# Performance work log

Hardware: AMD Instinct MI355X
Metric: run time of the kernel (lower is better)

Reference implementation:

```python
import jax, jax.numpy as jnp
import numpy as np

V, E, R, L = 50257, 256, 1024, 4
B, T = 32, 512
LN_EPS = 1e-5


def setup_inputs() -> dict:
    key = jax.random.key(0)
    ks = jax.random.split(key, 6)
    x = jax.random.randint(ks[0], (B, T), 0, V)
    embed = jax.random.normal(ks[1], (V, E), dtype=jnp.float32)
    # torch init: randn(in, out) / sqrt(in) / 0.9
    Win0 = jax.random.normal(ks[2], (E, R), dtype=jnp.float32) / np.sqrt(E).astype(np.float32) / 0.9
    Win_rest = jax.random.normal(ks[3], (L - 1, R, R), dtype=jnp.float32) / np.sqrt(R).astype(np.float32) / 0.9
    R_stack = jax.random.normal(ks[4], (L, R, R), dtype=jnp.float32) / np.sqrt(R).astype(np.float32) / 0.9
    gamma = jnp.ones((R * L,), dtype=jnp.float32)
    beta = jnp.zeros((R * L,), dtype=jnp.float32)
    return {"x": x, "embed": embed, "Win0": Win0, "Win_rest": Win_rest,
            "R_stack": R_stack, "gamma": gamma, "beta": beta}


def _layer_norm(h, gamma, beta):
    mu = jnp.mean(h, axis=-1, keepdims=True)
    var = jnp.mean(jnp.square(h - mu), axis=-1, keepdims=True)
    return (h - mu) * jax.lax.rsqrt(var + LN_EPS) * gamma + beta


def reference(x, embed, Win0, Win_rest, R_stack, gamma, beta):
    # x: [B,T] int ids. deep_type='deep_esn': layer i>0 takes the *current-step*
    # state of layer i-1 as input; readout concatenates all layer states.
    xe = embed[x]                      # [B,T,E]
    xe = jnp.transpose(xe, (1, 0, 2))  # [T,B,E] for scan over time
    b = x.shape[0]
    n_layers = R_stack.shape[0]
    r = R_stack.shape[1]
    init = tuple(jnp.zeros((b, r), dtype=xe.dtype) for _ in range(n_layers))

    def step(states, emb_t):
        new_states = []
        inp = emb_t
        for i in range(n_layers):
            W = Win0 if i == 0 else Win_rest[i - 1]
            s = jnp.tanh(states[i] @ R_stack[i] + inp @ W)  # [B,R]
            new_states.append(s)
            inp = s  # deep stacking: feed updated state to next layer
        return tuple(new_states), None

    final_states, _ = jax.lax.scan(step, init, xe)
    h = jnp.concatenate(final_states, axis=-1)  # [B, R*L]
    return _layer_norm(h, gamma, beta)
```

## Files before the change

kernel.cpp:

```cpp
#include <hip/hip_runtime.h>
#include <math.h>


#define TT    512
#define RDIM  1024
#define EDIM  256
#define NL    4
#define BB    32
#define NBLK  256
#define JW    16
#define HDIM  (RDIM * NL)
#define NPAN  4
#define CSTRIDE 32

#define S_ELEMS   (2 * NL * NPAN * RDIM * 8)
#define FIN_ELEMS (BB * HDIM)

typedef float vf2 __attribute__((ext_vector_type(2)));
typedef float vf4 __attribute__((ext_vector_type(4)));

__device__ __forceinline__ float dpp_xor1(float x) {
    return __int_as_float(__builtin_amdgcn_mov_dpp(__float_as_int(x), 0xB1, 0xF, 0xF, true));
}
__device__ __forceinline__ float dpp_xor2(float x) {
    return __int_as_float(__builtin_amdgcn_mov_dpp(__float_as_int(x), 0x4E, 0xF, 0xF, true));
}

__device__ __forceinline__ void gload_sc(vf4& d, const void* p) {
    asm volatile("global_load_dwordx4 %0, %1, off sc0 sc1" : "=v"(d) : "v"(p));
}
__device__ __forceinline__ void gload_pl(vf4& d, const void* p) {
    asm volatile("global_load_dwordx4 %0, %1, off" : "=v"(d) : "v"(p));
}
__device__ __forceinline__ void vwait(int wn, vf4& r) {
    if (wn >= 7)      asm volatile("s_waitcnt vmcnt(7)" : "+v"(r));
    else if (wn == 6) asm volatile("s_waitcnt vmcnt(6)" : "+v"(r));
    else if (wn == 5) asm volatile("s_waitcnt vmcnt(5)" : "+v"(r));
    else if (wn == 4) asm volatile("s_waitcnt vmcnt(4)" : "+v"(r));
    else if (wn == 3) asm volatile("s_waitcnt vmcnt(3)" : "+v"(r));
    else if (wn == 2) asm volatile("s_waitcnt vmcnt(2)" : "+v"(r));
    else if (wn == 1) asm volatile("s_waitcnt vmcnt(1)" : "+v"(r));
    else              asm volatile("s_waitcnt vmcnt(0)" : "+v"(r));
}

__global__ void gather_kernel(const int* __restrict__ x,
                              const float* __restrict__ embed,
                              float* __restrict__ xe)
{
    __shared__ int   ids[BB];
    __shared__ float sh[BB * (EDIM + 1)];
    const int t = blockIdx.x, tid = threadIdx.x;
    if (tid < BB) ids[tid] = x[tid * TT + t];
    __syncthreads();
    for (int r = 0; r < BB; ++r)
        sh[r * (EDIM + 1) + tid] = embed[ids[r] * EDIM + tid];
    __syncthreads();
    for (int i = tid; i < NPAN * EDIM * 8; i += 256) {
        int p = i >> 11, k = (i >> 3) & (EDIM - 1), bo = i & 7;
        xe[(size_t)t * (NPAN * EDIM * 8) + i] = sh[(p * 8 + bo) * (EDIM + 1) + k];
    }
}

template<int KIN, bool SCIN>
__device__ __forceinline__ void tick_body(
    const float* __restrict__ Sown, const float* __restrict__ Sin,
    const float* __restrict__ Wlds,
    const int kh, const int lam, const int kq, const int bh,
    vf2 acc[4][8])
{
    constexpr int NOWN = RDIM / 64;
    constexpr int NIN  = KIN / 64;
    constexpr int NT   = NOWN + NIN;

    const vf4* ownp = (const vf4*)Sown;
    const vf4* inp  = (const vf4*)Sin;

    vf4 b[8];

    #pragma unroll
    for (int i = 0; i < 8; ++i)
        gload_sc(b[i], (const void*)(ownp + (size_t)(kh * NOWN + i) * 64 + lam));

    #pragma unroll
    for (int i = 0; i < NT; ++i) {
        vf4& br = b[i & 7];
        const int wn = (NT - 1 - i) < 7 ? (NT - 1 - i) : 7;
        vwait(wn, br);
        const vf4 v = br;
        if (i + 8 < NT) {
            const int n = i + 8;
            if (n < NOWN) {
                gload_sc(br, (const void*)(ownp + (size_t)(kh * NOWN + n) * 64 + lam));
            } else {
                const void* p = (const void*)(inp + (size_t)(kh * NIN + (n - NOWN)) * 64 + lam);
                if (SCIN) gload_sc(br, p);
                else      gload_pl(br, p);
            }
        }
        const int k = (i < NOWN) ? ((kh * NOWN + i) * 32 + kq)
                                 : (RDIM + (kh * NIN + (i - NOWN)) * 32 + kq);
        const float* wr = &Wlds[k * JW + bh * 8];
        float4 wo0 = *(const float4*)wr;
        float4 wo1 = *(const float4*)(wr + 4);
        vf2 wv[8];
        wv[0] = (vf2){wo0.x, wo0.y}; wv[1] = (vf2){wo0.z, wo0.w};
        wv[2] = (vf2){wo1.x, wo1.y}; wv[3] = (vf2){wo1.z, wo1.w};
        wv[4] = (vf2){dpp_xor1(wo0.x), dpp_xor1(wo0.y)};
        wv[5] = (vf2){dpp_xor1(wo0.z), dpp_xor1(wo0.w)};
        wv[6] = (vf2){dpp_xor1(wo1.x), dpp_xor1(wo1.y)};
        wv[7] = (vf2){dpp_xor1(wo1.z), dpp_xor1(wo1.w)};
        const float vv[4] = {v[0], v[1], v[2], v[3]};
        #pragma unroll
        for (int q = 0; q < 4; ++q) {
            vf2 s = {vv[q], vv[q]};
            #pragma unroll
            for (int jp = 0; jp < 8; ++jp) acc[q][jp] += s * wv[jp];
        }
    }
}

__global__ __launch_bounds__(512, 2) void reservoir_kernel(
    const float* __restrict__ Win0, const float* __restrict__ WinR,
    const float* __restrict__ Rst,  const float* __restrict__ xe,
    float* __restrict__ S, float* __restrict__ Fin,
    unsigned* __restrict__ cnt, unsigned* __restrict__ rel)
{
    __shared__ float Wlds[2048 * JW];
    __shared__ float Pbuf[NPAN * JW * 8];
    const int tid   = threadIdx.x;
    const int blk   = blockIdx.x;
    const int layer = blk >> 6;
    const int j0    = (blk & 63) * JW;
    const int Kin   = (layer == 0) ? EDIM : RDIM;

    for (int idx = tid; idx < (RDIM + Kin) * JW; idx += 512) {
        int k = idx >> 4, j = idx & 15;
        float wv;
        if (k < RDIM) wv = Rst[((size_t)layer * RDIM + k) * RDIM + j0 + j];
        else {
            int k2 = k - RDIM;
            wv = (layer == 0) ? Win0[(size_t)k2 * RDIM + j0 + j]
                              : WinR[((size_t)(layer - 1) * RDIM + k2) * RDIM + j0 + j];
        }
        Wlds[idx] = wv;
    }
    __syncthreads();

    const int w8  = tid >> 6;
    const int w   = w8 & 3;
    const int kh  = w8 >> 2;
    const int lam = tid & 63;
    const int kq  = lam >> 1;
    const int bh  = lam & 1;
    const int bh4 = bh * 4;

    for (int tick = 0; tick < TT + NL - 1; ++tick) {
        const int t = tick - layer;
        if (t >= 0 && t < TT) {
            const int cur = tick & 1, prv = (tick - 1) & 1;
            const float* Sown = S + (((size_t)(prv * NL + layer)) * NPAN + w) * RDIM * 8;
            const float* Sin  = (layer == 0)
                ? (xe + ((size_t)t * NPAN + w) * (EDIM * 8))
                : (S + (((size_t)(prv * NL + layer - 1)) * NPAN + w) * RDIM * 8);

            vf2 acc[4][8];
            #pragma unroll
            for (int i = 0; i < 4; ++i)
                #pragma unroll
                for (int jp = 0; jp < 8; ++jp) acc[i][jp] = (vf2)(0.f);

            if (layer == 0) tick_body<EDIM, false>(Sown, Sin, Wlds, kh, lam, kq, bh, acc);
            else            tick_body<RDIM, true >(Sown, Sin, Wlds, kh, lam, kq, bh, acc);

            float r64v[64];
            #pragma unroll
            for (int i = 0; i < 4; ++i)
                #pragma unroll
                for (int jp = 0; jp < 8; ++jp) {
                    r64v[(i << 4) | (jp << 1)]     = acc[i][jp].x;
                    r64v[(i << 4) | (jp << 1) | 1] = acc[i][jp].y;
                }
            float r32v[32], r16v[16], r8v[8], r4v[4], rfin[2];
            {   const bool myb = kq & 1;
                #pragma unroll
                for (int m = 0; m < 32; ++m) {
                    float a = r64v[2 * m], b = r64v[2 * m + 1];
                    float send = myb ? a : b, keep = myb ? b : a;
                    r32v[m] = keep + dpp_xor2(send);
                }
            }
            {   const bool myb = (kq >> 1) & 1;
                #pragma unroll
                for (int m = 0; m < 16; ++m) {
                    float a = r32v[2 * m], b = r32v[2 * m + 1];
                    float send = myb ? a : b, keep = myb ? b : a;
                    r16v[m] = keep + __shfl_xor(send, 4, 64);
                }
            }
            {   const bool myb = (kq >> 2) & 1;
                #pragma unroll
                for (int m = 0; m < 8; ++m) {
                    float a = r16v[2 * m], b = r16v[2 * m + 1];
                    float send = myb ? a : b, keep = myb ? b : a;
                    r8v[m] = keep + __shfl_xor(send, 8, 64);
                }
            }
            {   const bool myb = (kq >> 3) & 1;
                #pragma unroll
                for (int m = 0; m < 4; ++m) {
                    float a = r8v[2 * m], b = r8v[2 * m + 1];
                    float send = myb ? a : b, keep = myb ? b : a;
                    r4v[m] = keep + __shfl_xor(send, 16, 64);
                }
            }
            {   const bool myb = (kq >> 4) & 1;
                #pragma unroll
                for (int m = 0; m < 2; ++m) {
                    float a = r4v[2 * m], b = r4v[2 * m + 1];
                    float send = myb ? a : b, keep = myb ? b : a;
                    rfin[m] = keep + __shfl_xor(send, 32, 64);
                }
            }

            const int i0 = kq >> 4;
            const int cc = kq & 15;
            const int j  = (cc & 7) + 8 * (bh ^ (cc >> 3));
            if (kh) {
                #pragma unroll
                for (int m = 0; m < 2; ++m)
                    Pbuf[(w * JW + j) * 8 + (bh4 + i0 + 2 * m)] = rfin[m];
            }
            __syncthreads();
            if (!kh) {
                float* sbase = S + (((size_t)(cur * NL + layer)) * NPAN + w) * RDIM * 8
                                 + (size_t)(j0 + j) * 8;
                #pragma unroll
                for (int m = 0; m < 2; ++m) {
                    const int bi = bh4 + i0 + 2 * m;
                    const float o = tanhf(rfin[m] + Pbuf[(w * JW + j) * 8 + bi]);
                    __hip_atomic_store(sbase + bi, o, __ATOMIC_RELAXED, __HIP_MEMORY_SCOPE_AGENT);
                    if (t == TT - 1)
                        Fin[(size_t)(w * 8 + bi) * HDIM + layer * RDIM + j0 + j] = o;
                }
            }
        }
        __syncthreads();
        if (tid == 0)
            __hip_atomic_fetch_add(&cnt[(blk & 15) * CSTRIDE], 1u,
                                   __ATOMIC_RELAXED, __HIP_MEMORY_SCOPE_AGENT);
        const unsigned wrel = (unsigned)(tick + 1);
        if (blk == 0) {
            if (tid < 64) {
                const unsigned wsum = wrel * (unsigned)NBLK;
                int guard = 0;
                for (;;) {
                    unsigned v = 0;
                    if (lam < 16)
                        v = __hip_atomic_load(&cnt[lam * CSTRIDE],
                                              __ATOMIC_RELAXED, __HIP_MEMORY_SCOPE_AGENT);
                    #pragma unroll
                    for (int m = 1; m <= 32; m <<= 1) v += __shfl_xor(v, m, 64);
                    if (v >= wsum) break;
                    __builtin_amdgcn_s_sleep(2);
                    if (++guard > (1 << 16)) break;
                }
                if (lam < 16)
                    __hip_atomic_store(&rel[lam * CSTRIDE], wrel,
                                       __ATOMIC_RELAXED, __HIP_MEMORY_SCOPE_AGENT);
            }
        } else {
            if (tid == 0) {
                int guard = 0;
                while (__hip_atomic_load(&rel[(blk & 15) * CSTRIDE],
                                         __ATOMIC_RELAXED, __HIP_MEMORY_SCOPE_AGENT) < wrel) {
                    __builtin_amdgcn_s_sleep(4);
                    if (++guard > (1 << 16)) break;
                }
            }
        }
        __syncthreads();
    }
}

__global__ void ln_kernel(const float* __restrict__ Fin,
                          const float* __restrict__ gamma,
                          const float* __restrict__ beta,
                          float* __restrict__ out)
{
    const int r = blockIdx.x, tid = threadIdx.x;
    const float* row = Fin + (size_t)r * HDIM;
    float s = 0.f, s2 = 0.f;
    for (int i = tid; i < HDIM; i += 256) { float v = row[i]; s += v; s2 += v * v; }
    for (int off = 32; off; off >>= 1) {
        s  += __shfl_down(s,  off, 64);
        s2 += __shfl_down(s2, off, 64);
    }
    __shared__ float rs[4], rs2[4];
    __shared__ float mu_s, rstd_s;
    if ((tid & 63) == 0) { rs[tid >> 6] = s; rs2[tid >> 6] = s2; }
    __syncthreads();
    if (tid == 0) {
        float S1 = rs[0] + rs[1] + rs[2] + rs[3];
        float S2 = rs2[0] + rs2[1] + rs2[2] + rs2[3];
        float mu = S1 / (float)HDIM;
        float var = S2 / (float)HDIM - mu * mu;
        mu_s = mu; rstd_s = rsqrtf(var + 1e-5f);
    }
    __syncthreads();
    float mu = mu_s, rstd = rstd_s;
    for (int i = tid; i < HDIM; i += 256)
        out[(size_t)r * HDIM + i] = (row[i] - mu) * rstd * gamma[i] + beta[i];
}

extern "C" void kernel_launch(void* const* d_in, const int* in_sizes, int n_in,
                              void* d_out, int out_size, void* d_ws, size_t ws_size,
                              hipStream_t stream)
{
    const int*   x     = (const int*)d_in[0];
    const float* embed = (const float*)d_in[1];
    const float* Win0  = (const float*)d_in[2];
    const float* WinR  = (const float*)d_in[3];
    const float* Rst   = (const float*)d_in[4];
    const float* gamma = (const float*)d_in[5];
    const float* beta  = (const float*)d_in[6];
    float* out = (float*)d_out;

    char* ws = (char*)d_ws;
    unsigned* cnt = (unsigned*)ws;
    unsigned* rel = cnt + 16 * CSTRIDE;
    float* S   = (float*)(ws + 8192);
    float* Fin = S + S_ELEMS;
    float* xe  = Fin + FIN_ELEMS;

    hipMemsetAsync(ws, 0, 8192 + (size_t)S_ELEMS * 4, stream);
    gather_kernel   <<<TT,   256, 0, stream>>>(x, embed, xe);
    reservoir_kernel<<<NBLK, 512, 0, stream>>>(Win0, WinR, Rst, xe, S, Fin, cnt, rel);
    ln_kernel       <<<BB,   256, 0, stream>>>(Fin, gamma, beta, out);
}
```

Measured before the change: 4.840 ms.

## Split each layer's work into recurrent and input K-segments across block pairs

Each block previously computed 16 output columns over the full K (recurrent plus input). Now pairs of blocks each own 32 columns: one block handles the recurrent R segment and the other the input W segment. The input-segment block publishes its partial sums to global memory with a per-tick flag, and the recurrent block waits on that flag, adds the partials and applies tanh. This halves the weight footprint per block in LDS and balances K-work, at the cost of an extra global handoff and spin-wait inside every tick.

```diff
diff --git a/kernel.cpp b/kernel.cpp
--- a/kernel.cpp
+++ b/kernel.cpp
@@ -8,12 +8,13 @@
 #define NL    4
 #define BB    32
 #define NBLK  256
-#define JW    16
+#define JW    32
 #define HDIM  (RDIM * NL)
 #define NPAN  4
 #define CSTRIDE 32
 
 #define S_ELEMS   (2 * NL * NPAN * RDIM * 8)
+#define PG_ELEMS  (NL * 32 * JW * BB)
 #define FIN_ELEMS (BB * HDIM)
 
 typedef float vf2 __attribute__((ext_vector_type(2)));
@@ -61,60 +62,122 @@
     }
 }
 
-template<int KIN, bool SCIN>
+template<int NI, bool SCIN>
 __device__ __forceinline__ void tick_body(
-    const float* __restrict__ Sown, const float* __restrict__ Sin,
-    const float* __restrict__ Wlds,
+    const float* __restrict__ Ssrc, const float* __restrict__ Wlds,
     const int kh, const int lam, const int kq, const int bh,
-    vf2 acc[4][8])
-{
-    constexpr int NOWN = RDIM / 64;
-    constexpr int NIN  = KIN / 64;
-    constexpr int NT   = NOWN + NIN;
-
-    const vf4* ownp = (const vf4*)Sown;
-    const vf4* inp  = (const vf4*)Sin;
-
+    vf2 acc0[4][8], vf2 acc1[4][8])
+{
+    const vf4* sp = (const vf4*)Ssrc;
     vf4 b[8];
+    constexpr int PRO = (NI < 8) ? NI : 8;
 
     #pragma unroll
-    for (int i = 0; i < 8; ++i)
-        gload_sc(b[i], (const void*)(ownp + (size_t)(kh * NOWN + i) * 64 + lam));
+    for (int i = 0; i < PRO; ++i) {
+        const void* p = (const void*)(sp + (size_t)(kh * NI + i) * 64 + lam);
+        if (SCIN) gload_sc(b[i], p); else gload_pl(b[i], p);
+    }
 
     #pragma unroll
-    for (int i = 0; i < NT; ++i) {
+    for (int i = 0; i < NI; ++i) {
         vf4& br = b[i & 7];
-        const int wn = (NT - 1 - i) < 7 ? (NT - 1 - i) : 7;
+        const int wn = (NI - 1 - i) < 7 ? (NI - 1 - i) : 7;
         vwait(wn, br);
         const vf4 v = br;
-        if (i + 8 < NT) {
-            const int n = i + 8;
-            if (n < NOWN) {
-                gload_sc(br, (const void*)(ownp + (size_t)(kh * NOWN + n) * 64 + lam));
-            } else {
-                const void* p = (const void*)(inp + (size_t)(kh * NIN + (n - NOWN)) * 64 + lam);
-                if (SCIN) gload_sc(br, p);
-                else      gload_pl(br, p);
-            }
-        }
-        const int k = (i < NOWN) ? ((kh * NOWN + i) * 32 + kq)
-                                 : (RDIM + (kh * NIN + (i - NOWN)) * 32 + kq);
-        const float* wr = &Wlds[k * JW + bh * 8];
-        float4 wo0 = *(const float4*)wr;
-        float4 wo1 = *(const float4*)(wr + 4);
-        vf2 wv[8];
-        wv[0] = (vf2){wo0.x, wo0.y}; wv[1] = (vf2){wo0.z, wo0.w};
-        wv[2] = (vf2){wo1.x, wo1.y}; wv[3] = (vf2){wo1.z, wo1.w};
-        wv[4] = (vf2){dpp_xor1(wo0.x), dpp_xor1(wo0.y)};
-        wv[5] = (vf2){dpp_xor1(wo0.z), dpp_xor1(wo0.w)};
-        wv[6] = (vf2){dpp_xor1(wo1.x), dpp_xor1(wo1.y)};
-        wv[7] = (vf2){dpp_xor1(wo1.z), dpp_xor1(wo1.w)};
+        if (i + 8 < NI) {
+            const void* p = (const void*)(sp + (size_t)(kh * NI + i + 8) * 64 + lam);
+            if (SCIN) gload_sc(br, p); else gload_pl(br, p);
+        }
+        const int krow = (kh * NI + i) * 32 + kq;
+        const float* wr = &Wlds[krow * JW];
         const float vv[4] = {v[0], v[1], v[2], v[3]};
-        #pragma unroll
-        for (int q = 0; q < 4; ++q) {
-            vf2 s = {vv[q], vv[q]};
+        {
+            float4 a0 = *(const float4*)(wr + bh * 8);
+            float4 a1 = *(const float4*)(wr + bh * 8 + 4);
+            vf2 wv[8];
+            wv[0] = (vf2){a0.x, a0.y}; wv[1] = (vf2){a0.z, a0.w};
+            wv[2] = (vf2){a1.x, a1.y}; wv[3] = (vf2){a1.z, a1.w};
+            wv[4] = (vf2){dpp_xor1(a0.x), dpp_xor1(a0.y)};
+            wv[5] = (vf2){dpp_xor1(a0.z), dpp_xor1(a0.w)};
+            wv[6] = (vf2){dpp_xor1(a1.x), dpp_xor1(a1.y)};
+            wv[7] = (vf2){dpp_xor1(a1.z), dpp_xor1(a1.w)};
             #pragma unroll
-            for (int jp = 0; jp < 8; ++jp) acc[q][jp] += s * wv[jp];
+            for (int q = 0; q < 4; ++q) {
+                vf2 s = {vv[q], vv[q]};
+                #pragma unroll
+                for (int jp = 0; jp < 8; ++jp) acc0[q][jp] += s * wv[jp];
+            }
+        }
+        {
+            float4 c0 = *(const float4*)(wr + 16 + bh * 8);
+            float4 c1 = *(const float4*)(wr + 16 + bh * 8 + 4);
+            vf2 wv[8];
+            wv[0] = (vf2){c0.x, c0.y}; wv[1] = (vf2){c0.z, c0.w};
+            wv[2] = (vf2){c1.x, c1.y}; wv[3] = (vf2){c1.z, c1.w};
+            wv[4] = (vf2){dpp_xor1(c0.x), dpp_xor1(c0.y)};
+            wv[5] = (vf2){dpp_xor1(c0.z), dpp_xor1(c0.w)};
+            wv[6] = (vf2){dpp_xor1(c1.x), dpp_xor1(c1.y)};
+            wv[7] = (vf2){dpp_xor1(c1.z), dpp_xor1(c1.w)};
+            #pragma unroll
+            for (int q = 0; q < 4; ++q) {
+                vf2 s = {vv[q], vv[q]};
+                #pragma unroll
+                for (int jp = 0; jp < 8; ++jp) acc1[q][jp] += s * wv[jp];
+            }
+        }
+    }
+}
+
+__device__ __forceinline__ void reduce64(const vf2 acc[4][8], const int kq,
+                                         float rfin[2])
+{
+    float r64v[64];
+    #pragma unroll
+    for (int i = 0; i < 4; ++i)
+        #pragma unroll
+        for (int jp = 0; jp < 8; ++jp) {
+            r64v[(i << 4) | (jp << 1)]     = acc[i][jp].x;
+            r64v[(i << 4) | (jp << 1) | 1] = acc[i][jp].y;
+        }
+    float r32v[32], r16v[16], r8v[8], r4v[4];
+    {   const bool myb = kq & 1;
+        #pragma unroll
+        for (int m = 0; m < 32; ++m) {
+            float a = r64v[2 * m], b = r64v[2 * m + 1];
+            float send = myb ? a : b, keep = myb ? b : a;
+            r32v[m] = keep + dpp_xor2(send);
+        }
+    }
+    {   const bool myb = (kq >> 1) & 1;
+        #pragma unroll
+        for (int m = 0; m < 16; ++m) {
+            float a = r32v[2 * m], b = r32v[2 * m + 1];
+            float send = myb ? a : b, keep = myb ? b : a;
+            r16v[m] = keep + __shfl_xor(send, 4, 64);
+        }
+    }
+    {   const bool myb = (kq >> 2) & 1;
+        #pragma unroll
+        for (int m = 0; m < 8; ++m) {
+            float a = r16v[2 * m], b = r16v[2 * m + 1];
+            float send = myb ? a : b, keep = myb ? b : a;
+            r8v[m] = keep + __shfl_xor(send, 8, 64);
+        }
+    }
+    {   const bool myb = (kq >> 3) & 1;
+        #pragma unroll
+        for (int m = 0; m < 4; ++m) {
+            float a = r8v[2 * m], b = r8v[2 * m + 1];
+            float send = myb ? a : b, keep = myb ? b : a;
+            r4v[m] = keep + __shfl_xor(send, 16, 64);
+        }
+    }
+    {   const bool myb = (kq >> 4) & 1;
+        #pragma unroll
+        for (int m = 0; m < 2; ++m) {
+            float a = r4v[2 * m], b = r4v[2 * m + 1];
+            float send = myb ? a : b, keep = myb ? b : a;
+            rfin[m] = keep + __shfl_xor(send, 32, 64);
         }
     }
 }
@@ -122,26 +185,27 @@
 __global__ __launch_bounds__(512, 2) void reservoir_kernel(
     const float* __restrict__ Win0, const float* __restrict__ WinR,
     const float* __restrict__ Rst,  const float* __restrict__ xe,
-    float* __restrict__ S, float* __restrict__ Fin,
-    unsigned* __restrict__ cnt, unsigned* __restrict__ rel)
-{
-    __shared__ float Wlds[2048 * JW];
+    float* __restrict__ S, float* __restrict__ Pglob, float* __restrict__ Fin,
+    unsigned* __restrict__ cnt, unsigned* __restrict__ rel,
+    unsigned* __restrict__ flagP)
+{
+    __shared__ float Wlds[RDIM * JW];
     __shared__ float Pbuf[NPAN * JW * 8];
     const int tid   = threadIdx.x;
     const int blk   = blockIdx.x;
     const int layer = blk >> 6;
-    const int j0    = (blk & 63) * JW;
-    const int Kin   = (layer == 0) ? EDIM : RDIM;
-
-    for (int idx = tid; idx < (RDIM + Kin) * JW; idx += 512) {
-        int k = idx >> 4, j = idx & 15;
+    const int r     = blk & 63;
+    const int seg   = r >> 5;
+    const int g     = r & 31;
+    const int j0    = g * JW;
+    const int KSEG  = (seg == 0) ? RDIM : (layer == 0 ? EDIM : RDIM);
+
+    for (int idx = tid; idx < KSEG * JW; idx += 512) {
+        int k = idx >> 5, j = idx & 31;
         float wv;
-        if (k < RDIM) wv = Rst[((size_t)layer * RDIM + k) * RDIM + j0 + j];
-        else {
-            int k2 = k - RDIM;
-            wv = (layer == 0) ? Win0[(size_t)k2 * RDIM + j0 + j]
-                              : WinR[((size_t)(layer - 1) * RDIM + k2) * RDIM + j0 + j];
-        }
+        if (seg == 0) wv = Rst[((size_t)layer * RDIM + k) * RDIM + j0 + j];
+        else          wv = (layer == 0) ? Win0[(size_t)k * RDIM + j0 + j]
+                                        : WinR[((size_t)(layer - 1) * RDIM + k) * RDIM + j0 + j];
         Wlds[idx] = wv;
     }
     __syncthreads();
@@ -153,94 +217,106 @@
     const int kq  = lam >> 1;
     const int bh  = lam & 1;
     const int bh4 = bh * 4;
+    const int pgi = layer * 32 + g;
+    float* const pg = Pglob + (size_t)pgi * (JW * BB);
 
     for (int tick = 0; tick < TT + NL - 1; ++tick) {
         const int t = tick - layer;
         if (t >= 0 && t < TT) {
             const int cur = tick & 1, prv = (tick - 1) & 1;
-            const float* Sown = S + (((size_t)(prv * NL + layer)) * NPAN + w) * RDIM * 8;
-            const float* Sin  = (layer == 0)
-                ? (xe + ((size_t)t * NPAN + w) * (EDIM * 8))
-                : (S + (((size_t)(prv * NL + layer - 1)) * NPAN + w) * RDIM * 8);
-
-            vf2 acc[4][8];
-            #pragma unroll
-            for (int i = 0; i < 4; ++i)
-                #pragma unroll
-                for (int jp = 0; jp < 8; ++jp) acc[i][jp] = (vf2)(0.f);
-
-            if (layer == 0) tick_body<EDIM, false>(Sown, Sin, Wlds, kh, lam, kq, bh, acc);
-            else            tick_body<RDIM, true >(Sown, Sin, Wlds, kh, lam, kq, bh, acc);
-
-            float r64v[64];
+
+            vf2 acc0[4][8], acc1[4][8];
             #pragma unroll
             for (int i = 0; i < 4; ++i)
                 #pragma unroll
                 for (int jp = 0; jp < 8; ++jp) {
-                    r64v[(i << 4) | (jp << 1)]     = acc[i][jp].x;
-                    r64v[(i << 4) | (jp << 1) | 1] = acc[i][jp].y;
-                }
-            float r32v[32], r16v[16], r8v[8], r4v[4], rfin[2];
-            {   const bool myb = kq & 1;
-                #pragma unroll
-                for (int m = 0; m < 32; ++m) {
-                    float a = r64v[2 * m], b = r64v[2 * m + 1];
-                    float send = myb ? a : b, keep = myb ? b : a;
-                    r32v[m] = keep + dpp_xor2(send);
-                }
-            }
-            {   const bool myb = (kq >> 1) & 1;
-                #pragma unroll
-                for (int m = 0; m < 16; ++m) {
-                    float a = r32v[2 * m], b = r32v[2 * m + 1];
-                    float send = myb ? a : b, keep = myb ? b : a;
-                    r16v[m] = keep + __shfl_xor(send, 4, 64);
-                }
-            }
-            {   const bool myb = (kq >> 2) & 1;
-                #pragma unroll
-                for (int m = 0; m < 8; ++m) {
-                    float a = r16v[2 * m], b = r16v[2 * m + 1];
-                    float send = myb ? a : b, keep = myb ? b : a;
-                    r8v[m] = keep + __shfl_xor(send, 8, 64);
-                }
-            }
-            {   const bool myb = (kq >> 3) & 1;
-                #pragma unroll
-                for (int m = 0; m < 4; ++m) {
-                    float a = r8v[2 * m], b = r8v[2 * m + 1];
-                    float send = myb ? a : b, keep = myb ? b : a;
-                    r4v[m] = keep + __shfl_xor(send, 16, 64);
-                }
-            }
-            {   const bool myb = (kq >> 4) & 1;
+                    acc0[i][jp] = (vf2)(0.f); acc1[i][jp] = (vf2)(0.f);
+                }
+
+            if (seg == 0) {
+                const float* Ssrc = S + (((size_t)(prv * NL + layer)) * NPAN + w) * RDIM * 8;
+                tick_body<16, true>(Ssrc, Wlds, kh, lam, kq, bh, acc0, acc1);
+            } else if (layer == 0) {
+                const float* Ssrc = xe + ((size_t)t * NPAN + w) * (EDIM * 8);
+                tick_body<4, false>(Ssrc, Wlds, kh, lam, kq, bh, acc0, acc1);
+            } else {
+                const float* Ssrc = S + (((size_t)(prv * NL + layer - 1)) * NPAN + w) * RDIM * 8;
+                tick_body<16, true>(Ssrc, Wlds, kh, lam, kq, bh, acc0, acc1);
+            }
+
+            float rf0[2], rf1[2];
+            reduce64(acc0, kq, rf0);
+            reduce64(acc1, kq, rf1);
+
+            const int i0 = kq >> 4;
+            const int cc = kq & 15;
+            const int jb = (cc & 7) + 8 * (bh ^ (cc >> 3));
+            if (kh) {
                 #pragma unroll
                 for (int m = 0; m < 2; ++m) {
-                    float a = r4v[2 * m], b = r4v[2 * m + 1];
-                    float send = myb ? a : b, keep = myb ? b : a;
-                    rfin[m] = keep + __shfl_xor(send, 32, 64);
-                }
-            }
-
-            const int i0 = kq >> 4;
-            const int cc = kq & 15;
-            const int j  = (cc & 7) + 8 * (bh ^ (cc >> 3));
-            if (kh) {
-                #pragma unroll
-                for (int m = 0; m < 2; ++m)
-                    Pbuf[(w * JW + j) * 8 + (bh4 + i0 + 2 * m)] = rfin[m];
+                    Pbuf[(w * JW + jb) * 8 + (bh4 + i0 + 2 * m)]      = rf0[m];
+                    Pbuf[(w * JW + 16 + jb) * 8 + (bh4 + i0 + 2 * m)] = rf1[m];
+                }
             }
             __syncthreads();
-            if (!kh) {
-                float* sbase = S + (((size_t)(cur * NL + layer)) * NPAN + w) * RDIM * 8
-                                 + (size_t)(j0 + j) * 8;
-                #pragma unroll
-                for (int m = 0; m < 2; ++m) {
-                    const int bi = bh4 + i0 + 2 * m;
-                    const float o = tanhf(rfin[m] + Pbuf[(w * JW + j) * 8 + bi]);
-                    __hip_atomic_store(sbase + bi, o, __ATOMIC_RELAXED, __HIP_MEMORY_SCOPE_AGENT);
-                    if (t == TT - 1)
-                        Fin[(size_t)(w * 8 + bi) * HDIM + layer * RDIM + j0 + j] = o;
+
+            if (seg == 1) {
+                if (!kh) {
+                    #pragma unroll
+                    for (int m = 0; m < 2; ++m) {
+                        const int bi = bh4 + i0 + 2 * m;
+                        float p0 = rf0[m] + Pbuf[(w * JW + jb) * 8 + bi];
+                        float p1 = rf1[m] + Pbuf[(w * JW + 16 + jb) * 8 + bi];
+                        __hip_atomic_store(&pg[(size_t)jb * BB + w * 8 + bi], p0,
+                                           __ATOMIC_RELAXED, __HIP_MEMORY_SCOPE_AGENT);
+                        __hip_atomic_store(&pg[(size_t)(16 + jb) * BB + w * 8 + bi], p1,
+                                           __ATOMIC_RELAXED, __HIP_MEMORY_SCOPE_AGENT);
+                    }
+                }
+                __syncthreads();
+                if (tid == 0)
+                    __hip_atomic_store(&flagP[pgi * CSTRIDE], (unsigned)(tick + 1),
+                                       __ATOMIC_RELAXED, __HIP_MEMORY_SCOPE_AGENT);
+            } else {
+                if (tid == 0) {
+                    int guard = 0;
+                    while (__hip_atomic_load(&flagP[pgi * CSTRIDE],
+                                             __ATOMIC_RELAXED, __HIP_MEMORY_SCOPE_AGENT)
+                           < (unsigned)(tick + 1)) {
+                        __builtin_amdgcn_s_sleep(2);
+                        if (++guard > (1 << 18)) break;
+                    }
+                }
+                __syncthreads();
+                if (!kh) {
+                    float v0[2], v1[2], q0[2], q1[2];
+                    #pragma unroll
+                    for (int m = 0; m < 2; ++m) {
+                        const int bi = bh4 + i0 + 2 * m;
+                        v0[m] = rf0[m] + Pbuf[(w * JW + jb) * 8 + bi];
+                        v1[m] = rf1[m] + Pbuf[(w * JW + 16 + jb) * 8 + bi];
+                        q0[m] = __uint_as_float(__hip_atomic_load(
+                                  (const unsigned*)&pg[(size_t)jb * BB + w * 8 + bi],
+                                  __ATOMIC_RELAXED, __HIP_MEMORY_SCOPE_AGENT));
+                        q1[m] = __uint_as_float(__hip_atomic_load(
+                                  (const unsigned*)&pg[(size_t)(16 + jb) * BB + w * 8 + bi],
+                                  __ATOMIC_RELAXED, __HIP_MEMORY_SCOPE_AGENT));
+                    }
+                    float* sbase = S + (((size_t)(cur * NL + layer)) * NPAN + w) * RDIM * 8;
+                    #pragma unroll
+                    for (int m = 0; m < 2; ++m) {
+                        const int bi = bh4 + i0 + 2 * m;
+                        const float o0 = tanhf(v0[m] + q0[m]);
+                        const float o1 = tanhf(v1[m] + q1[m]);
+                        __hip_atomic_store(sbase + (size_t)(j0 + jb) * 8 + bi, o0,
+                                           __ATOMIC_RELAXED, __HIP_MEMORY_SCOPE_AGENT);
+                        __hip_atomic_store(sbase + (size_t)(j0 + 16 + jb) * 8 + bi, o1,
+                                           __ATOMIC_RELAXED, __HIP_MEMORY_SCOPE_AGENT);
+                        if (t == TT - 1) {
+                            Fin[(size_t)(w * 8 + bi) * HDIM + layer * RDIM + j0 + jb]      = o0;
+                            Fin[(size_t)(w * 8 + bi) * HDIM + layer * RDIM + j0 + 16 + jb] = o1;
+                        }
+                    }
                 }
             }
         }
@@ -326,14 +402,17 @@
     float* out = (float*)d_out;
 
     char* ws = (char*)d_ws;
-    unsigned* cnt = (unsigned*)ws;
-    unsigned* rel = cnt + 16 * CSTRIDE;
-    float* S   = (float*)(ws + 8192);
-    float* Fin = S + S_ELEMS;
-    float* xe  = Fin + FIN_ELEMS;
-
-    hipMemsetAsync(ws, 0, 8192 + (size_t)S_ELEMS * 4, stream);
+    unsigned* cnt   = (unsigned*)ws;
+    unsigned* rel   = cnt + 16 * CSTRIDE;
+    unsigned* flagP = (unsigned*)(ws + 4096);
+    float* S     = (float*)(ws + 24576);
+    float* Pglob = S + S_ELEMS;
+    float* Fin   = Pglob + PG_ELEMS;
+    float* xe    = Fin + FIN_ELEMS;
+
+    hipMemsetAsync(ws, 0, 24576 + (size_t)S_ELEMS * 4, stream);
     gather_kernel   <<<TT,   256, 0, stream>>>(x, embed, xe);
-    reservoir_kernel<<<NBLK, 512, 0, stream>>>(Win0, WinR, Rst, xe, S, Fin, cnt, rel);
+    reservoir_kernel<<<NBLK, 512, 0, stream>>>(Win0, WinR, Rst, xe, S, Pglob, Fin,
+                                               cnt, rel, flagP);
     ln_kernel       <<<BB,   256, 0, stream>>>(Fin, gamma, beta, out);
 }
```

Result: slower. 5.977 ms (+23.5%).

## Split reservoir columns across 512 persistent blocks with 8-column tiles

Applied to the files above, without the earlier changes.

Halves the column tile per block from 16 to 8 and doubles the grid to 512 persistent blocks at launch bound 4 blocks per SM, so each block does half the FMA work per tick. The reduction tree is rewritten for 32 partials and the dpp lane-swap of weights is removed. Each block still streams the full state vectors every tick, so total global/L2 read traffic doubles, and the grid barrier must now gather twice as many arrivals. It also relies on all 512 blocks being co-resident.

```diff
diff --git a/kernel.cpp b/kernel.cpp
--- a/kernel.cpp
+++ b/kernel.cpp
@@ -7,8 +7,8 @@
 #define EDIM  256
 #define NL    4
 #define BB    32
-#define NBLK  256
-#define JW    16
+#define NBLK  512
+#define JW    8
 #define HDIM  (RDIM * NL)
 #define NPAN  4
 #define CSTRIDE 32
@@ -19,9 +19,6 @@
 typedef float vf2 __attribute__((ext_vector_type(2)));
 typedef float vf4 __attribute__((ext_vector_type(4)));
 
-__device__ __forceinline__ float dpp_xor1(float x) {
-    return __int_as_float(__builtin_amdgcn_mov_dpp(__float_as_int(x), 0xB1, 0xF, 0xF, true));
-}
 __device__ __forceinline__ float dpp_xor2(float x) {
     return __int_as_float(__builtin_amdgcn_mov_dpp(__float_as_int(x), 0x4E, 0xF, 0xF, true));
 }
@@ -61,16 +58,15 @@
     }
 }
 
-template<int KIN, bool SCIN>
+template<int NI, bool SCIN>
 __device__ __forceinline__ void tick_body(
     const float* __restrict__ Sown, const float* __restrict__ Sin,
     const float* __restrict__ Wlds,
-    const int kh, const int lam, const int kq, const int bh,
-    vf2 acc[4][8])
-{
-    constexpr int NOWN = RDIM / 64;
-    constexpr int NIN  = KIN / 64;
-    constexpr int NT   = NOWN + NIN;
+    const int kh, const int lam, const int kq,
+    vf2 acc[4][4])
+{
+    constexpr int NOWN = 16;
+    constexpr int NT   = NOWN + NI;
 
     const vf4* ownp = (const vf4*)Sown;
     const vf4* inp  = (const vf4*)Sin;
@@ -92,34 +88,81 @@
             if (n < NOWN) {
                 gload_sc(br, (const void*)(ownp + (size_t)(kh * NOWN + n) * 64 + lam));
             } else {
-                const void* p = (const void*)(inp + (size_t)(kh * NIN + (n - NOWN)) * 64 + lam);
+                const void* p = (const void*)(inp + (size_t)(kh * NI + (n - NOWN)) * 64 + lam);
                 if (SCIN) gload_sc(br, p);
                 else      gload_pl(br, p);
             }
         }
-        const int k = (i < NOWN) ? ((kh * NOWN + i) * 32 + kq)
-                                 : (RDIM + (kh * NIN + (i - NOWN)) * 32 + kq);
-        const float* wr = &Wlds[k * JW + bh * 8];
-        float4 wo0 = *(const float4*)wr;
-        float4 wo1 = *(const float4*)(wr + 4);
-        vf2 wv[8];
-        wv[0] = (vf2){wo0.x, wo0.y}; wv[1] = (vf2){wo0.z, wo0.w};
-        wv[2] = (vf2){wo1.x, wo1.y}; wv[3] = (vf2){wo1.z, wo1.w};
-        wv[4] = (vf2){dpp_xor1(wo0.x), dpp_xor1(wo0.y)};
-        wv[5] = (vf2){dpp_xor1(wo0.z), dpp_xor1(wo0.w)};
-        wv[6] = (vf2){dpp_xor1(wo1.x), dpp_xor1(wo1.y)};
-        wv[7] = (vf2){dpp_xor1(wo1.z), dpp_xor1(wo1.w)};
+        const int krow = (i < NOWN) ? ((kh * NOWN + i) * 32 + kq)
+                                    : (RDIM + (kh * NI + (i - NOWN)) * 32 + kq);
+        const float* wr = &Wlds[krow * JW];
+        float4 a0 = *(const float4*)wr;
+        float4 a1 = *(const float4*)(wr + 4);
+        vf2 wv[4];
+        wv[0] = (vf2){a0.x, a0.y}; wv[1] = (vf2){a0.z, a0.w};
+        wv[2] = (vf2){a1.x, a1.y}; wv[3] = (vf2){a1.z, a1.w};
         const float vv[4] = {v[0], v[1], v[2], v[3]};
         #pragma unroll
         for (int q = 0; q < 4; ++q) {
             vf2 s = {vv[q], vv[q]};
             #pragma unroll
-            for (int jp = 0; jp < 8; ++jp) acc[q][jp] += s * wv[jp];
-        }
-    }
-}
-
-__global__ __launch_bounds__(512, 2) void reservoir_kernel(
+            for (int jp = 0; jp < 4; ++jp) acc[q][jp] += s * wv[jp];
+        }
+    }
+}
+
+__device__ __forceinline__ float reduce32(const vf2 acc[4][4], const int kq)
+{
+    float r32v[32];
+    #pragma unroll
+    for (int q = 0; q < 4; ++q)
+        #pragma unroll
+        for (int jp = 0; jp < 4; ++jp) {
+            r32v[(q << 3) | (jp << 1)]     = acc[q][jp].x;
+            r32v[(q << 3) | (jp << 1) | 1] = acc[q][jp].y;
+        }
+    float r16v[16], r8v[8], r4v[4], r2v[2], rfin;
+    {   const bool myb = kq & 1;
+        #pragma unroll
+        for (int m = 0; m < 16; ++m) {
+            float a = r32v[2 * m], b = r32v[2 * m + 1];
+            float send = myb ? a : b, keep = myb ? b : a;
+            r16v[m] = keep + dpp_xor2(send);
+        }
+    }
+    {   const bool myb = (kq >> 1) & 1;
+        #pragma unroll
+        for (int m = 0; m < 8; ++m) {
+            float a = r16v[2 * m], b = r16v[2 * m + 1];
+            float send = myb ? a : b, keep = myb ? b : a;
+            r8v[m] = keep + __shfl_xor(send, 4, 64);
+        }
+    }
+    {   const bool myb = (kq >> 2) & 1;
+        #pragma unroll
+        for (int m = 0; m < 4; ++m) {
+            float a = r8v[2 * m], b = r8v[2 * m + 1];
+            float send = myb ? a : b, keep = myb ? b : a;
+            r4v[m] = keep + __shfl_xor(send, 8, 64);
+        }
+    }
+    {   const bool myb = (kq >> 3) & 1;
+        #pragma unroll
+        for (int m = 0; m < 2; ++m) {
+            float a = r4v[2 * m], b = r4v[2 * m + 1];
+            float send = myb ? a : b, keep = myb ? b : a;
+            r2v[m] = keep + __shfl_xor(send, 16, 64);
+        }
+    }
+    {   const bool myb = (kq >> 4) & 1;
+        float a = r2v[0], b = r2v[1];
+        float send = myb ? a : b, keep = myb ? b : a;
+        rfin = keep + __shfl_xor(send, 32, 64);
+    }
+    return rfin;
+}
+
+__global__ __launch_bounds__(512, 4) void reservoir_kernel(
     const float* __restrict__ Win0, const float* __restrict__ WinR,
     const float* __restrict__ Rst,  const float* __restrict__ xe,
     float* __restrict__ S, float* __restrict__ Fin,
@@ -129,12 +172,13 @@
     __shared__ float Pbuf[NPAN * JW * 8];
     const int tid   = threadIdx.x;
     const int blk   = blockIdx.x;
-    const int layer = blk >> 6;
-    const int j0    = (blk & 63) * JW;
+    const int layer = blk >> 7;
+    const int g     = blk & 127;
+    const int j0    = g * JW;
     const int Kin   = (layer == 0) ? EDIM : RDIM;
 
     for (int idx = tid; idx < (RDIM + Kin) * JW; idx += 512) {
-        int k = idx >> 4, j = idx & 15;
+        int k = idx >> 3, j = idx & 7;
         float wv;
         if (k < RDIM) wv = Rst[((size_t)layer * RDIM + k) * RDIM + j0 + j];
         else {
@@ -152,7 +196,8 @@
     const int lam = tid & 63;
     const int kq  = lam >> 1;
     const int bh  = lam & 1;
-    const int bh4 = bh * 4;
+    const int col = 2 * (2 * ((kq >> 2) & 1) + ((kq >> 1) & 1)) + (kq & 1);
+    const int bi  = bh * 4 + 2 * ((kq >> 4) & 1) + ((kq >> 3) & 1);
 
     for (int tick = 0; tick < TT + NL - 1; ++tick) {
         const int t = tick - layer;
@@ -163,85 +208,27 @@
                 ? (xe + ((size_t)t * NPAN + w) * (EDIM * 8))
                 : (S + (((size_t)(prv * NL + layer - 1)) * NPAN + w) * RDIM * 8);
 
-            vf2 acc[4][8];
+            vf2 acc[4][4];
             #pragma unroll
             for (int i = 0; i < 4; ++i)
                 #pragma unroll
-                for (int jp = 0; jp < 8; ++jp) acc[i][jp] = (vf2)(0.f);
-
-            if (layer == 0) tick_body<EDIM, false>(Sown, Sin, Wlds, kh, lam, kq, bh, acc);
-            else            tick_body<RDIM, true >(Sown, Sin, Wlds, kh, lam, kq, bh, acc);
-
-            float r64v[64];
-            #pragma unroll
-            for (int i = 0; i < 4; ++i)
-                #pragma unroll
-                for (int jp = 0; jp < 8; ++jp) {
-                    r64v[(i << 4) | (jp << 1)]     = acc[i][jp].x;
-                    r64v[(i << 4) | (jp << 1) | 1] = acc[i][jp].y;
-                }
-            float r32v[32], r16v[16], r8v[8], r4v[4], rfin[2];
-            {   const bool myb = kq & 1;
-                #pragma unroll
-                for (int m = 0; m < 32; ++m) {
-                    float a = r64v[2 * m], b = r64v[2 * m + 1];
-                    float send = myb ? a : b, keep = myb ? b : a;
-                    r32v[m] = keep + dpp_xor2(send);
-                }
-            }
-            {   const bool myb = (kq >> 1) & 1;
-                #pragma unroll
-                for (int m = 0; m < 16; ++m) {
-                    float a = r32v[2 * m], b = r32v[2 * m + 1];
-                    float send = myb ? a : b, keep = myb ? b : a;
-                    r16v[m] = keep + __shfl_xor(send, 4, 64);
-                }
-            }
-            {   const bool myb = (kq >> 2) & 1;
-                #pragma unroll
-                for (int m = 0; m < 8; ++m) {
-                    float a = r16v[2 * m], b = r16v[2 * m + 1];
-                    float send = myb ? a : b, keep = myb ? b : a;
-                    r8v[m] = keep + __shfl_xor(send, 8, 64);
-                }
-            }
-            {   const bool myb = (kq >> 3) & 1;
-                #pragma unroll
-                for (int m = 0; m < 4; ++m) {
-                    float a = r8v[2 * m], b = r8v[2 * m + 1];
-                    float send = myb ? a : b, keep = myb ? b : a;
-                    r4v[m] = keep + __shfl_xor(send, 16, 64);
-                }
-            }
-            {   const bool myb = (kq >> 4) & 1;
-                #pragma unroll
-                for (int m = 0; m < 2; ++m) {
-                    float a = r4v[2 * m], b = r4v[2 * m + 1];
-                    float send = myb ? a : b, keep = myb ? b : a;
-                    rfin[m] = keep + __shfl_xor(send, 32, 64);
-                }
-            }
-
-            const int i0 = kq >> 4;
-            const int cc = kq & 15;
-            const int j  = (cc & 7) + 8 * (bh ^ (cc >> 3));
-            if (kh) {
-                #pragma unroll
-                for (int m = 0; m < 2; ++m)
-                    Pbuf[(w * JW + j) * 8 + (bh4 + i0 + 2 * m)] = rfin[m];
-            }
+                for (int jp = 0; jp < 4; ++jp) acc[i][jp] = (vf2)(0.f);
+
+            if (layer == 0) tick_body<4,  false>(Sown, Sin, Wlds, kh, lam, kq, acc);
+            else            tick_body<16, true >(Sown, Sin, Wlds, kh, lam, kq, acc);
+
+            const float rf = reduce32(acc, kq);
+
+            if (kh)
+                Pbuf[(w * JW + col) * 8 + bi] = rf;
             __syncthreads();
             if (!kh) {
-                float* sbase = S + (((size_t)(cur * NL + layer)) * NPAN + w) * RDIM * 8
-                                 + (size_t)(j0 + j) * 8;
-                #pragma unroll
-                for (int m = 0; m < 2; ++m) {
-                    const int bi = bh4 + i0 + 2 * m;
-                    const float o = tanhf(rfin[m] + Pbuf[(w * JW + j) * 8 + bi]);
-                    __hip_atomic_store(sbase + bi, o, __ATOMIC_RELAXED, __HIP_MEMORY_SCOPE_AGENT);
-                    if (t == TT - 1)
-                        Fin[(size_t)(w * 8 + bi) * HDIM + layer * RDIM + j0 + j] = o;
-                }
+                const float o = tanhf(rf + Pbuf[(w * JW + col) * 8 + bi]);
+                float* sdst = S + (((size_t)(cur * NL + layer)) * NPAN + w) * RDIM * 8
+                                + (size_t)(j0 + col) * 8 + bi;
+                __hip_atomic_store(sdst, o, __ATOMIC_RELAXED, __HIP_MEMORY_SCOPE_AGENT);
+                if (t == TT - 1)
+                    Fin[(size_t)(w * 8 + bi) * HDIM + layer * RDIM + j0 + col] = o;
             }
         }
         __syncthreads();
@@ -262,7 +249,7 @@
                     for (int m = 1; m <= 32; m <<= 1) v += __shfl_xor(v, m, 64);
                     if (v >= wsum) break;
                     __builtin_amdgcn_s_sleep(2);
-                    if (++guard > (1 << 16)) break;
+                    if (++guard > (1 << 17)) break;
                 }
                 if (lam < 16)
                     __hip_atomic_store(&rel[lam * CSTRIDE], wrel,
@@ -274,7 +261,7 @@
                 while (__hip_atomic_load(&rel[(blk & 15) * CSTRIDE],
                                          __ATOMIC_RELAXED, __HIP_MEMORY_SCOPE_AGENT) < wrel) {
                     __builtin_amdgcn_s_sleep(4);
-                    if (++guard > (1 << 16)) break;
+                    if (++guard > (1 << 17)) break;
                 }
             }
         }
```

New measurement: 5.171 ms. 6.8% more time.

## Split K across four wave groups with 1024-thread blocks in reservoir kernel

Applied to the files above, without the earlier changes.

Doubles the threads per block from 512 to 1024 and splits the reduction dimension four ways instead of two. Each lane now loads dwordx2 state chunks and accumulates half as many batch columns, which removes the DPP weight swizzle and one shuffle-reduction stage. Partial sums from the three extra K-groups go through a larger LDS buffer and are summed before tanh. The aim is to shorten the serial per-tick latency of the persistent recurrent loop by using more waves per tick. The cost is more LDS traffic and heavier block-wide syncs, and 1024 threads may limit per-thread register budget.

```diff
diff --git a/kernel.cpp b/kernel.cpp
--- a/kernel.cpp
+++ b/kernel.cpp
@@ -11,28 +11,23 @@
 #define JW    16
 #define HDIM  (RDIM * NL)
 #define NPAN  4
+#define NKH   4
 #define CSTRIDE 32
 
 #define S_ELEMS   (2 * NL * NPAN * RDIM * 8)
 #define FIN_ELEMS (BB * HDIM)
 
 typedef float vf2 __attribute__((ext_vector_type(2)));
-typedef float vf4 __attribute__((ext_vector_type(4)));
-
-__device__ __forceinline__ float dpp_xor1(float x) {
-    return __int_as_float(__builtin_amdgcn_mov_dpp(__float_as_int(x), 0xB1, 0xF, 0xF, true));
-}
-__device__ __forceinline__ float dpp_xor2(float x) {
-    return __int_as_float(__builtin_amdgcn_mov_dpp(__float_as_int(x), 0x4E, 0xF, 0xF, true));
-}
-
-__device__ __forceinline__ void gload_sc(vf4& d, const void* p) {
-    asm volatile("global_load_dwordx4 %0, %1, off sc0 sc1" : "=v"(d) : "v"(p));
-}
-__device__ __forceinline__ void gload_pl(vf4& d, const void* p) {
-    asm volatile("global_load_dwordx4 %0, %1, off" : "=v"(d) : "v"(p));
-}
-__device__ __forceinline__ void vwait(int wn, vf4& r) {
+
+typedef unsigned long long ull;
+
+__device__ __forceinline__ void gload2_sc(vf2& d, const void* p) {
+    asm volatile("global_load_dwordx2 %0, %1, off sc0 sc1" : "=v"(d) : "v"(p));
+}
+__device__ __forceinline__ void gload2_pl(vf2& d, const void* p) {
+    asm volatile("global_load_dwordx2 %0, %1, off" : "=v"(d) : "v"(p));
+}
+__device__ __forceinline__ void vwait2(int wn, vf2& r) {
     if (wn >= 7)      asm volatile("s_waitcnt vmcnt(7)" : "+v"(r));
     else if (wn == 6) asm volatile("s_waitcnt vmcnt(6)" : "+v"(r));
     else if (wn == 5) asm volatile("s_waitcnt vmcnt(5)" : "+v"(r));
@@ -61,79 +56,138 @@
     }
 }
 
-template<int KIN, bool SCIN>
+template<int NI, bool SCIN>
 __device__ __forceinline__ void tick_body(
     const float* __restrict__ Sown, const float* __restrict__ Sin,
     const float* __restrict__ Wlds,
-    const int kh, const int lam, const int kq, const int bh,
-    vf2 acc[4][8])
-{
-    constexpr int NOWN = RDIM / 64;
-    constexpr int NIN  = KIN / 64;
-    constexpr int NT   = NOWN + NIN;
-
-    const vf4* ownp = (const vf4*)Sown;
-    const vf4* inp  = (const vf4*)Sin;
-
-    vf4 b[8];
+    const int k4, const int kq, const int bq,
+    vf2 acc[2][8])
+{
+    constexpr int NOWN = 16;
+    constexpr int NT   = NOWN + NI;
+
+    const ull* ownp = (const ull*)Sown;
+    const ull* inp  = (const ull*)Sin;
+    const int obase = k4 * 1024 + kq * 4 + bq;
+    const int ibase = k4 * (NI * 64) + kq * 4 + bq;
+
+    vf2 b[8];
 
     #pragma unroll
     for (int i = 0; i < 8; ++i)
-        gload_sc(b[i], (const void*)(ownp + (size_t)(kh * NOWN + i) * 64 + lam));
+        gload2_sc(b[i], (const void*)(ownp + obase + i * 64));
 
     #pragma unroll
     for (int i = 0; i < NT; ++i) {
-        vf4& br = b[i & 7];
+        vf2& br = b[i & 7];
         const int wn = (NT - 1 - i) < 7 ? (NT - 1 - i) : 7;
-        vwait(wn, br);
-        const vf4 v = br;
+        vwait2(wn, br);
+        const vf2 v = br;
         if (i + 8 < NT) {
             const int n = i + 8;
             if (n < NOWN) {
-                gload_sc(br, (const void*)(ownp + (size_t)(kh * NOWN + n) * 64 + lam));
+                gload2_sc(br, (const void*)(ownp + obase + n * 64));
             } else {
-                const void* p = (const void*)(inp + (size_t)(kh * NIN + (n - NOWN)) * 64 + lam);
-                if (SCIN) gload_sc(br, p);
-                else      gload_pl(br, p);
-            }
-        }
-        const int k = (i < NOWN) ? ((kh * NOWN + i) * 32 + kq)
-                                 : (RDIM + (kh * NIN + (i - NOWN)) * 32 + kq);
-        const float* wr = &Wlds[k * JW + bh * 8];
-        float4 wo0 = *(const float4*)wr;
-        float4 wo1 = *(const float4*)(wr + 4);
-        vf2 wv[8];
-        wv[0] = (vf2){wo0.x, wo0.y}; wv[1] = (vf2){wo0.z, wo0.w};
-        wv[2] = (vf2){wo1.x, wo1.y}; wv[3] = (vf2){wo1.z, wo1.w};
-        wv[4] = (vf2){dpp_xor1(wo0.x), dpp_xor1(wo0.y)};
-        wv[5] = (vf2){dpp_xor1(wo0.z), dpp_xor1(wo0.w)};
-        wv[6] = (vf2){dpp_xor1(wo1.x), dpp_xor1(wo1.y)};
-        wv[7] = (vf2){dpp_xor1(wo1.z), dpp_xor1(wo1.w)};
-        const float vv[4] = {v[0], v[1], v[2], v[3]};
-        #pragma unroll
-        for (int q = 0; q < 4; ++q) {
-            vf2 s = {vv[q], vv[q]};
+                const void* p = (const void*)(inp + ibase + (n - NOWN) * 64);
+                if (SCIN) gload2_sc(br, p);
+                else      gload2_pl(br, p);
+            }
+        }
+        const int wrow = (i < NOWN) ? (k4 * 256 + i * 16 + kq)
+                                    : (RDIM + k4 * (NI * 16) + (i - NOWN) * 16 + kq);
+        const float* wr = &Wlds[wrow * JW];
+        const float vv[2] = {v.x, v.y};
+        {
+            float4 a0 = *(const float4*)wr;
+            float4 a1 = *(const float4*)(wr + 4);
+            vf2 wv[4];
+            wv[0] = (vf2){a0.x, a0.y}; wv[1] = (vf2){a0.z, a0.w};
+            wv[2] = (vf2){a1.x, a1.y}; wv[3] = (vf2){a1.z, a1.w};
             #pragma unroll
-            for (int jp = 0; jp < 8; ++jp) acc[q][jp] += s * wv[jp];
-        }
-    }
-}
-
-__global__ __launch_bounds__(512, 2) void reservoir_kernel(
+            for (int q = 0; q < 2; ++q) {
+                vf2 s = {vv[q], vv[q]};
+                #pragma unroll
+                for (int jp = 0; jp < 4; ++jp) acc[q][jp] += s * wv[jp];
+            }
+        }
+        {
+            float4 c0 = *(const float4*)(wr + 8);
+            float4 c1 = *(const float4*)(wr + 12);
+            vf2 wv[4];
+            wv[0] = (vf2){c0.x, c0.y}; wv[1] = (vf2){c0.z, c0.w};
+            wv[2] = (vf2){c1.x, c1.y}; wv[3] = (vf2){c1.z, c1.w};
+            #pragma unroll
+            for (int q = 0; q < 2; ++q) {
+                vf2 s = {vv[q], vv[q]};
+                #pragma unroll
+                for (int jp = 0; jp < 4; ++jp) acc[q][4 + jp] += s * wv[jp];
+            }
+        }
+    }
+}
+
+__device__ __forceinline__ void reduce32q(const vf2 acc[2][8], const int kq,
+                                          float rfin[2])
+{
+    float r32v[32];
+    #pragma unroll
+    for (int i = 0; i < 2; ++i)
+        #pragma unroll
+        for (int jp = 0; jp < 8; ++jp) {
+            r32v[(i << 4) | (jp << 1)]     = acc[i][jp].x;
+            r32v[(i << 4) | (jp << 1) | 1] = acc[i][jp].y;
+        }
+    float r16v[16], r8v[8], r4v[4];
+    {   const bool myb = kq & 1;
+        #pragma unroll
+        for (int m = 0; m < 16; ++m) {
+            float a = r32v[2 * m], b = r32v[2 * m + 1];
+            float send = myb ? a : b, keep = myb ? b : a;
+            r16v[m] = keep + __shfl_xor(send, 4, 64);
+        }
+    }
+    {   const bool myb = (kq >> 1) & 1;
+        #pragma unroll
+        for (int m = 0; m < 8; ++m) {
+            float a = r16v[2 * m], b = r16v[2 * m + 1];
+            float send = myb ? a : b, keep = myb ? b : a;
+            r8v[m] = keep + __shfl_xor(send, 8, 64);
+        }
+    }
+    {   const bool myb = (kq >> 2) & 1;
+        #pragma unroll
+        for (int m = 0; m < 4; ++m) {
+            float a = r8v[2 * m], b = r8v[2 * m + 1];
+            float send = myb ? a : b, keep = myb ? b : a;
+            r4v[m] = keep + __shfl_xor(send, 16, 64);
+        }
+    }
+    {   const bool myb = (kq >> 3) & 1;
+        #pragma unroll
+        for (int m = 0; m < 2; ++m) {
+            float a = r4v[2 * m], b = r4v[2 * m + 1];
+            float send = myb ? a : b, keep = myb ? b : a;
+            rfin[m] = keep + __shfl_xor(send, 32, 64);
+        }
+    }
+}
+
+__global__ __launch_bounds__(1024) void reservoir_kernel(
     const float* __restrict__ Win0, const float* __restrict__ WinR,
     const float* __restrict__ Rst,  const float* __restrict__ xe,
     float* __restrict__ S, float* __restrict__ Fin,
     unsigned* __restrict__ cnt, unsigned* __restrict__ rel)
 {
     __shared__ float Wlds[2048 * JW];
-    __shared__ float Pbuf[NPAN * JW * 8];
+    __shared__ float Pbuf[(NKH - 1) * NPAN * JW * 8];
     const int tid   = threadIdx.x;
     const int blk   = blockIdx.x;
     const int layer = blk >> 6;
-    const int j0    = (blk & 63) * JW;
+    const int g     = blk & 63;
+    const int j0    = g * JW;
     const int Kin   = (layer == 0) ? EDIM : RDIM;
 
-    for (int idx = tid; idx < (RDIM + Kin) * JW; idx += 512) {
+    for (int idx = tid; idx < (RDIM + Kin) * JW; idx += 1024) {
         int k = idx >> 4, j = idx & 15;
         float wv;
         if (k < RDIM) wv = Rst[((size_t)layer * RDIM + k) * RDIM + j0 + j];
@@ -146,13 +200,12 @@
     }
     __syncthreads();
 
-    const int w8  = tid >> 6;
-    const int w   = w8 & 3;
-    const int kh  = w8 >> 2;
+    const int w16 = tid >> 6;
+    const int w   = w16 & 3;
+    const int k4  = w16 >> 2;
     const int lam = tid & 63;
-    const int kq  = lam >> 1;
-    const int bh  = lam & 1;
-    const int bh4 = bh * 4;
+    const int kq  = lam >> 2;
+    const int bq  = lam & 3;
 
     for (int tick = 0; tick < TT + NL - 1; ++tick) {
         const int t = tick - layer;
@@ -163,84 +216,38 @@
                 ? (xe + ((size_t)t * NPAN + w) * (EDIM * 8))
                 : (S + (((size_t)(prv * NL + layer - 1)) * NPAN + w) * RDIM * 8);
 
-            vf2 acc[4][8];
+            vf2 acc[2][8];
             #pragma unroll
-            for (int i = 0; i < 4; ++i)
+            for (int i = 0; i < 2; ++i)
                 #pragma unroll
                 for (int jp = 0; jp < 8; ++jp) acc[i][jp] = (vf2)(0.f);
 
-            if (layer == 0) tick_body<EDIM, false>(Sown, Sin, Wlds, kh, lam, kq, bh, acc);
-            else            tick_body<RDIM, true >(Sown, Sin, Wlds, kh, lam, kq, bh, acc);
-
-            float r64v[64];
-            #pragma unroll
-            for (int i = 0; i < 4; ++i)
-                #pragma unroll
-                for (int jp = 0; jp < 8; ++jp) {
-                    r64v[(i << 4) | (jp << 1)]     = acc[i][jp].x;
-                    r64v[(i << 4) | (jp << 1) | 1] = acc[i][jp].y;
-                }
-            float r32v[32], r16v[16], r8v[8], r4v[4], rfin[2];
-            {   const bool myb = kq & 1;
-                #pragma unroll
-                for (int m = 0; m < 32; ++m) {
-                    float a = r64v[2 * m], b = r64v[2 * m + 1];
-                    float send = myb ? a : b, keep = myb ? b : a;
-                    r32v[m] = keep + dpp_xor2(send);
-                }
-            }
-            {   const bool myb = (kq >> 1) & 1;
-                #pragma unroll
-                for (int m = 0; m < 16; ++m) {
-                    float a = r32v[2 * m], b = r32v[2 * m + 1];
-                    float send = myb ? a : b, keep = myb ? b : a;
-                    r16v[m] = keep + __shfl_xor(send, 4, 64);
-                }
-            }
-            {   const bool myb = (kq >> 2) & 1;
-                #pragma unroll
-                for (int m = 0; m < 8; ++m) {
-                    float a = r16v[2 * m], b = r16v[2 * m + 1];
-                    float send = myb ? a : b, keep = myb ? b : a;
-                    r8v[m] = keep + __shfl_xor(send, 8, 64);
-                }
-            }
-            {   const bool myb = (kq >> 3) & 1;
-                #pragma unroll
-                for (int m = 0; m < 4; ++m) {
-                    float a = r8v[2 * m], b = r8v[2 * m + 1];
-                    float send = myb ? a : b, keep = myb ? b : a;
-                    r4v[m] = keep + __shfl_xor(send, 16, 64);
-                }
-            }
-            {   const bool myb = (kq >> 4) & 1;
+            if (layer == 0) tick_body<4,  false>(Sown, Sin, Wlds, k4, kq, bq, acc);
+            else            tick_body<16, true >(Sown, Sin, Wlds, k4, kq, bq, acc);
+
+            float rfin[2];
+            reduce32q(acc, kq, rfin);
+
+            if (k4) {
+                #pragma unroll
+                for (int m = 0; m < 2; ++m)
+                    Pbuf[((((k4 - 1) * NPAN + w) * JW + kq) << 3) + bq * 2 + m] = rfin[m];
+            }
+            __syncthreads();
+            if (!k4) {
+                float* sbase = S + (((size_t)(cur * NL + layer)) * NPAN + w) * RDIM * 8
+                                 + (size_t)(j0 + kq) * 8;
                 #pragma unroll
                 for (int m = 0; m < 2; ++m) {
-                    float a = r4v[2 * m], b = r4v[2 * m + 1];
-                    float send = myb ? a : b, keep = myb ? b : a;
-                    rfin[m] = keep + __shfl_xor(send, 32, 64);
-                }
-            }
-
-            const int i0 = kq >> 4;
-            const int cc = kq & 15;
-            const int j  = (cc & 7) + 8 * (bh ^ (cc >> 3));
-            if (kh) {
-                #pragma unroll
-                for (int m = 0; m < 2; ++m)
-                    Pbuf[(w * JW + j) * 8 + (bh4 + i0 + 2 * m)] = rfin[m];
-            }
-            __syncthreads();
-            if (!kh) {
-                float* sbase = S + (((size_t)(cur * NL + layer)) * NPAN + w) * RDIM * 8
-                                 + (size_t)(j0 + j) * 8;
-                #pragma unroll
-                for (int m = 0; m < 2; ++m) {
-                    const int bi = bh4 + i0 + 2 * m;
-                    const float o = tanhf(rfin[m] + Pbuf[(w * JW + j) * 8 + bi]);
+                    const int bi = bq * 2 + m;
+                    float v = rfin[m];
+                    #pragma unroll
+                    for (int q = 1; q < NKH; ++q)
+                        v += Pbuf[((((q - 1) * NPAN + w) * JW + kq) << 3) + bi];
+                    const float o = tanhf(v);
                     __hip_atomic_store(sbase + bi, o, __ATOMIC_RELAXED, __HIP_MEMORY_SCOPE_AGENT);
                     if (t == TT - 1)
-                        Fin[(size_t)(w * 8 + bi) * HDIM + layer * RDIM + j0 + j] = o;
+                        Fin[(size_t)(w * 8 + bi) * HDIM + layer * RDIM + j0 + kq] = o;
                 }
             }
         }
@@ -334,6 +341,6 @@
 
     hipMemsetAsync(ws, 0, 8192 + (size_t)S_ELEMS * 4, stream);
     gather_kernel   <<<TT,   256, 0, stream>>>(x, embed, xe);
-    reservoir_kernel<<<NBLK, 512, 0, stream>>>(Win0, WinR, Rst, xe, S, Fin, cnt, rel);
+    reservoir_kernel<<<NBLK, 1024, 0, stream>>>(Win0, WinR, Rst, xe, S, Fin, cnt, rel);
     ln_kernel       <<<BB,   256, 0, stream>>>(Fin, gamma, beta, out);
 }
```

Result: slower. 5.775 ms (+19.3%).
